# Performance work log

Measured on AMD Instinct MI355X. Metric: run time of the kernel, lower is better.

The kernel has to match this reference:

```python
import jax, jax.numpy as jnp
import numpy as np
from jax import lax

SHIFT = 32  # shift_range from init
EPS_NORM = 1e-12
EPS_MASK = 1e-6


def _l2_normalize_flat(x):
    # F.normalize(x.reshape(B,-1)): per-sample L2 normalize with eps 1e-12
    B = x.shape[0]
    flat = x.reshape(B, -1)
    n = jnp.linalg.norm(flat, axis=1, keepdims=True)
    return (flat / jnp.maximum(n, EPS_NORM)).reshape(x.shape)


def setup_inputs() -> dict:
    key = jax.random.key(0)
    k1, k2 = jax.random.split(key)
    grd_feature = jax.random.normal(k1, (8, 32, 32, 32), dtype=jnp.float32)
    sat_feature = jax.random.normal(k2, (8, 32, 128, 128), dtype=jnp.float32)
    return {"grd_feature": grd_feature, "sat_feature": sat_feature, "test_method": 1}


def reference(grd_feature, sat_feature, test_method):
    # test_method == 1 path (default); test_method in {0,1} only differ in divisor
    M, C, H_s, W_s = sat_feature.shape
    N, _, H, W = grd_feature.shape
    kH = min(H, H_s - 2 * SHIFT)
    kW = min(W, W_s - 2 * SHIFT)

    # center-crop ground template to (kH, kW) and L2-normalize per sample
    gh0, gw0 = H // 2 - kH // 2, W // 2 - kW // 2
    grd = grd_feature[:, :, gh0:gh0 + 2 * (kH // 2), gw0:gw0 + 2 * (kW // 2)]
    N_, _, H_k, W_k = grd.shape
    grd = _l2_normalize_flat(grd)

    # center-crop satellite to search region and L2-normalize per sample
    sh0 = H_s // 2 - SHIFT - kH // 2
    sw0 = W_s // 2 - SHIFT - kW // 2
    sat = sat_feature[:, :, sh0:sh0 + 2 * (SHIFT + kH // 2), sw0:sw0 + 2 * (SHIFT + kW // 2)]
    _, _, H_i, W_i = sat.shape
    sat = _l2_normalize_flat(sat)

    # all-pairs cross-correlation: corr[m, n, y, x] (torch grouped-conv on repeated sat
    # is equivalent to a plain VALID conv of sat with all N ground filters)
    corr = lax.conv_general_dilated(
        sat, grd, window_strides=(1, 1), padding='VALID',
        dimension_numbers=('NCHW', 'OIHW', 'NCHW'))  # [M, N, Ho, Wo]
    Ho, Wo = corr.shape[2], corr.shape[3]

    # sliding-window sum of |sat|^2 (avg_pool with divisor_override=1, summed over C)
    s2 = jnp.sum(sat * sat, axis=1)  # [M, H_i, W_i]
    partical = lax.reduce_window(s2, jnp.float32(0), lax.add,
                                 (1, H_k, W_k), (1, 1, 1), 'VALID')  # [M, Ho, Wo]
    if test_method == 0:
        denom = jnp.sqrt(partical)
    else:
        denom = partical
    corr = corr / jnp.maximum(denom[:, None], EPS_NORM)

    similarity_matrix = jnp.max(corr, axis=(2, 3))  # [M, N]

    # diagonal pairs (m == n): peak localization
    diag = jnp.diagonal(corr, axis1=0, axis2=1)        # [Ho, Wo, M]
    diag = jnp.transpose(diag, (2, 0, 1)).reshape(M, -1)
    max_index = jnp.argmax(diag, axis=-1)
    pos_h = max_index // Wo
    pos_w = max_index % Wo

    grd_mask = (jnp.abs(jnp.sum(grd, axis=1)) > EPS_MASK).astype(jnp.float32)  # [N, H_k, W_k]

    def place(ph, pw, gm):
        z = jnp.zeros((1, H_i, W_i), dtype=jnp.float32)
        return lax.dynamic_update_slice(z, gm[None], (0, ph, pw))

    mask = jax.vmap(place)(pos_h, pos_w, grd_mask)  # [M, 1, H_i, W_i]
    return similarity_matrix, mask
```

## Files before the change

### kernel.cpp

```cpp
#include <hip/hip_runtime.h>
#include <stdint.h>

typedef unsigned short u16;
typedef unsigned int u32;
typedef unsigned long long u64;
typedef __bf16 bf16x8 __attribute__((ext_vector_type(8)));
typedef float floatx4 __attribute__((ext_vector_type(4)));

#define DEVI static __device__ __forceinline__

DEVI u16 f2bf(float f) {
  uint32_t u = __builtin_bit_cast(uint32_t, f);
  u += 0x7FFFu + ((u >> 16) & 1u);
  return (u16)(u >> 16);
}
DEVI float bf2f(u16 b) { return __builtin_bit_cast(float, (uint32_t)b << 16); }

DEVI u32 encf(float f) {
  u32 u = __builtin_bit_cast(u32, f);
  return (u >> 31) ? ~u : (u | 0x80000000u);
}
DEVI float decf(u32 e) {
  u32 u = (e >> 31) ? (e & 0x7FFFFFFFu) : ~e;
  return __builtin_bit_cast(float, u);
}

DEVI float wred_sum(float v) {
  #pragma unroll
  for (int o = 32; o > 0; o >>= 1) v += __shfl_xor(v, o);
  return v;
}
DEVI float wred_max(float v) {
  #pragma unroll
  for (int o = 32; o > 0; o >>= 1) v = fmaxf(v, __shfl_xor(v, o));
  return v;
}

DEVI void cp16(const u16* g, u16* l) {
#if __has_builtin(__builtin_amdgcn_global_load_lds)
  __builtin_amdgcn_global_load_lds(
      (const __attribute__((address_space(1))) uint32_t*)g,
      (__attribute__((address_space(3))) uint32_t*)l, 16, 0, 0);
#else
  *(uint4*)l = *(const uint4*)g;
#endif
}

static constexpr size_t OFF_CORRP = 0;
static constexpr size_t OFF_SATT  = OFF_CORRP + (size_t)4*270400*4;
static constexpr size_t OFF_GRDP  = OFF_SATT + (size_t)8*4*96*96*8*2;
static constexpr size_t OFF_S2    = OFF_GRDP + (size_t)4*1024*16*8*2;
static constexpr size_t OFF_PART  = OFF_S2   + (size_t)73728*4;
static constexpr size_t OFF_NRMP  = OFF_PART + (size_t)33800*4;
static constexpr size_t OFF_GNRM  = OFF_NRMP + 768*4;
static constexpr size_t OFF_MASK  = OFF_GNRM + 32;
static constexpr size_t OFF_PMAX  = OFF_MASK + (size_t)8192*4;
static constexpr size_t OFF_CNT   = OFF_PMAX + 320*4;

__global__ __launch_bounds__(256) void k_prep(
    const float* __restrict__ grd, const float* __restrict__ sat,
    u16* __restrict__ sTh, u16* __restrict__ gP,
    float* __restrict__ s2, float* __restrict__ nrmp,
    float* __restrict__ gnrm, float* __restrict__ gmask,
    u32* __restrict__ cnts) {
  __shared__ float L[32*100];
  __shared__ float red[4];
  const int t = threadIdx.x;
  if (blockIdx.x < 768) {
    const int m = blockIdx.x / 96, y = blockIdx.x - (blockIdx.x / 96) * 96;
    #pragma unroll
    for (int k = 0; k < 3; ++k) {
      const int idx = k*256 + t;
      const int c = idx / 24, xq = idx - c*24;
      const float4 v = *(const float4*)(sat + (((size_t)m*32 + c)*128 + (16+y))*128 + 16 + xq*4);
      *(float4*)(&L[c*100 + xq*4]) = v;
    }
    __syncthreads();
    float ss = 0.f;
    if (t < 96) {
      #pragma unroll
      for (int c = 0; c < 32; ++c) { const float v = L[c*100 + t]; ss += v*v; }
      s2[(size_t)m*9216 + y*96 + t] = ss;
    }
    const float wsum = wred_sum(ss);
    if ((t & 63) == 0) red[t >> 6] = wsum;
    __syncthreads();
    if (t == 0) nrmp[m*96 + y] = red[0] + red[1] + red[2] + red[3];
    for (int idx = t; idx < 384; idx += 256) {
      const int cb = idx / 96, x = idx - cb*96;
      union { u16 us[8]; uint4 v4; } P;
      #pragma unroll
      for (int e = 0; e < 8; ++e) P.us[e] = f2bf(L[(cb*8+e)*100 + x]);
      *(uint4*)(&sTh[(((size_t)m*4+cb)*9216 + (size_t)y*96 + x)*8]) = P.v4;
    }
  } else if (blockIdx.x == 776) {
    if (t < 96) cnts[t] = (t == 72) ? 768u : 0u;
  } else {
    const int n = blockIdx.x - 768;
    float nn = 0.f, scs[4];
    #pragma unroll
    for (int it = 0; it < 4; ++it) {
      const int pidx = it*256 + t;
      float vals[32]; float sc = 0.f;
      #pragma unroll
      for (int c = 0; c < 32; ++c) {
        const float v = grd[((size_t)n*32 + c)*1024 + pidx];
        vals[c] = v; sc += v; nn += v*v;
      }
      scs[it] = sc;
      #pragma unroll
      for (int cb = 0; cb < 4; ++cb) {
        union { u16 us[8]; uint4 v4; } ph, pl;
        #pragma unroll
        for (int e = 0; e < 8; ++e) {
          const float v = vals[cb*8+e];
          const u16 h = f2bf(v); ph.us[e] = h; pl.us[e] = f2bf(v - bf2f(h));
        }
        const size_t o = ((size_t)cb*1024 + pidx)*128;
        *(uint4*)(&gP[o + (size_t)n*8])     = ph.v4;
        *(uint4*)(&gP[o + (size_t)(n+8)*8]) = pl.v4;
      }
    }
    const float tot = wred_sum(nn);
    if ((t & 63) == 0) red[t >> 6] = tot;
    __syncthreads();
    const float sum = red[0] + red[1] + red[2] + red[3];
    if (t == 0) gnrm[n] = sum;
    const float gn = fmaxf(sqrtf(sum), 1e-12f);
    const float thr = 1e-6f * gn;
    #pragma unroll
    for (int it = 0; it < 4; ++it)
      gmask[n*1024 + it*256 + t] = (fabsf(scs[it]) > thr) ? 1.f : 0.f;
  }
}

__global__ __launch_bounds__(256, 3) void k_conv(
    const u16* __restrict__ satT, const u16* __restrict__ gP,
    const float* __restrict__ s2, float* __restrict__ corr_p,
    float* __restrict__ part, u32* __restrict__ tick)
{
  __shared__ __align__(16) u16 patch[41*48*8];
  __shared__ u32 s_bi;

  const int tid = threadIdx.x;
  const int wave = tid >> 6, lane = tid & 63;
  const int pr = lane & 15, q = lane >> 4;

  u32 bi = blockIdx.x;
  for (;;) {
    if (bi < 72) {
      float* S  = (float*)patch;
      float* HS = S + 40*96;
      const int pm = (int)bi / 9, ysl = ((int)bi - pm*9)*8;
      const int nrows = (65 - ysl) < 8 ? (65 - ysl) : 8;
      const int scnt  = (96 - ysl) < 40 ? (96 - ysl) : 40;
      for (int idx = tid; idx < scnt*96; idx += 256)
        S[idx] = s2[(size_t)pm*9216 + (size_t)ysl*96 + idx];
      __syncthreads();
      const int hrows = nrows + 31;
      for (int idx = tid; idx < hrows*65; idx += 256) {
        const int r = idx / 65, xo = idx - r*65;
        const float* p = &S[r*96 + xo];
        float s = 0.f;
        #pragma unroll
        for (int j = 0; j < 32; ++j) s += p[j];
        HS[idx] = s;
      }
      __syncthreads();
      for (int idx = tid; idx < nrows*65; idx += 256) {
        const int r = idx / 65, xo = idx - r*65;
        float s = 0.f;
        #pragma unroll
        for (int i = 0; i < 32; ++i) s += HS[(r+i)*65 + xo];
        part[(size_t)pm*4225 + (size_t)(ysl+r)*65 + xo] = s;
      }
    } else if (bi >= 968) {
      const int e = (int)bi - 968;
      const int cb = e & 3;
      const int yt = (e >> 2) % 5;
      const int m  = e / 20;
      const int ybase = yt * 13;
      const size_t rowbase = ((size_t)(m*4 + cb) * 96 + ybase) * 96;
      for (int k = tid; k < 44*32; k += 256) {
        const int rho = k >> 5, px = k & 31;
        cp16(&satT[(rowbase + (size_t)rho*96 + 64 + px)*8], &patch[(size_t)k*8]);
      }
      asm volatile("s_waitcnt vmcnt(0)" ::: "memory");
      __syncthreads();
      const int prc = pr < 13 ? pr : 12;
      floatx4 acc = (floatx4){0.f, 0.f, 0.f, 0.f};
      #pragma unroll
      for (int jbi = 0; jbi < 2; ++jbi) {
        const int jb = wave*2 + jbi;
        const int px_e = jb*4 + q;
        const u16* bp = gP + ((size_t)cb*1024 + (size_t)(jb*4+q))*128 + (size_t)pr*8;
        uint4 Br[8];
        #pragma unroll
        for (int ii = 0; ii < 8; ++ii) Br[ii] = *(const uint4*)(bp + (size_t)ii*4096);
        uint4 Ah[8];
        #pragma unroll
        for (int s = 0; s < 6; ++s)
          Ah[s] = *(const uint4*)(&patch[((size_t)(prc + s)*32 + px_e)*8]);
        #pragma unroll
        for (int i = 0; i < 32; ++i) {
          if (i < 26)
            Ah[(i+6)&7] = *(const uint4*)(&patch[((size_t)(prc + i + 6)*32 + px_e)*8]);
          const bf16x8 bf = __builtin_bit_cast(bf16x8, Br[i&7]);
          if (i < 24)
            Br[(i+8)&7] = *(const uint4*)(bp + (size_t)(i+8)*4096);
          acc = __builtin_amdgcn_mfma_f32_16x16x32_bf16(
              __builtin_bit_cast(bf16x8, Ah[i&7]), bf, acc, 0, 0, 0);
        }
      }
      float v4[4];
      #pragma unroll
      for (int k = 0; k < 4; ++k) v4[k] = acc[k] + __shfl_xor(acc[k], 8);
      __syncthreads();
      float* red = (float*)patch;
      #pragma unroll
      for (int k = 0; k < 4; ++k) red[((size_t)wave*64 + lane)*5 + k] = v4[k];
      __syncthreads();
      if (wave == 0 && pr < 8) {
        #pragma unroll
        for (int k = 0; k < 4; ++k) {
          const int yoff = q*4 + k;
          if (yoff < 13) {
            float s = 0.f;
            #pragma unroll
            for (int w = 0; w < 4; ++w) s += red[((size_t)w*64 + lane)*5 + k];
            corr_p[(size_t)cb*270400 + ((size_t)(m*8+pr)*65 + (ybase+yoff))*65 + 64] = s;
          }
        }
      }
    } else {
      int bb = (int)bi - 72;
      const int cb = bb & 3; bb >>= 2;
      const int xt = bb & 3; bb >>= 2;
      const int yt = bb % 7;
      const int m  = bb / 7;
      const int x0 = xt*16;

      if (yt < 6) {
        const int y0 = yt*10;
        const size_t rowbase = ((size_t)(m*4 + cb) * 96 + y0) * 96;
        for (int k = tid; k < 41*48; k += 256) {
          const int rho = k / 48, px = k - (k/48)*48;
          cp16(&satT[(rowbase + (size_t)rho*96 + x0 + px)*8], &patch[(size_t)k*8]);
        }
        asm volatile("s_waitcnt vmcnt(0)" ::: "memory");
        __syncthreads();

        floatx4 acc[10];
        #pragma unroll
        for (int r = 0; r < 10; ++r) acc[r] = (floatx4){0.f, 0.f, 0.f, 0.f};

        #pragma unroll
        for (int jbi = 0; jbi < 2; ++jbi) {
          const int jb = wave*2 + jbi;
          const int apx = pr + jb*4 + q;
          const u16* bp = gP + ((size_t)cb*1024 + (size_t)(jb*4+q))*128 + (size_t)pr*8;

          uint4 Br[8];
          #pragma unroll
          for (int ii = 0; ii < 8; ++ii) Br[ii] = *(const uint4*)(bp + (size_t)ii*4096);
          uint4 Ah[12];
          #pragma unroll
          for (int s = 0; s < 12; ++s) Ah[s] = *(const uint4*)(&patch[((size_t)s*48 + apx)*8]);

          #pragma unroll
          for (int i = 0; i < 32; ++i) {
            const bf16x8 bf = __builtin_bit_cast(bf16x8, Br[i&7]);
            if (i < 24)
              Br[(i+8)&7] = *(const uint4*)(bp + (size_t)(i+8)*4096);
            __builtin_amdgcn_s_setprio(1);
            #pragma unroll
            for (int r = 0; r < 10; ++r)
              acc[r] = __builtin_amdgcn_mfma_f32_16x16x32_bf16(
                  __builtin_bit_cast(bf16x8, Ah[(i+r)%12]), bf, acc[r], 0, 0, 0);
            __builtin_amdgcn_s_setprio(0);
            if (i < 29)
              Ah[(i+12)%12] = *(const uint4*)(&patch[((size_t)(i+12)*48 + apx)*8]);
          }
        }

        float* red = (float*)patch;
        #pragma unroll
        for (int half = 0; half < 2; ++half) {
          __syncthreads();
          #pragma unroll
          for (int u = 0; u < 20; ++u)
            red[((size_t)wave*64 + lane)*21 + u] = acc[half*5 + (u>>2)][u&3];
          __syncthreads();
          if (pr < 8) {
            const int fw = wave;
            #pragma unroll
            for (int r = 0; r < 5; ++r) {
              float s = 0.f;
              #pragma unroll
              for (int w = 0; w < 4; ++w)
                s += red[((size_t)w*64 + lane)*21 + r*4 + fw]
                   + red[((size_t)w*64 + (lane^8))*21 + r*4 + fw];
              const int x = x0 + q*4 + fw;
              corr_p[(size_t)cb*270400 + ((size_t)(m*8+pr)*65 + (y0 + half*5 + r))*65 + x] = s;
            }
          }
        }
      } else {
        const int y0 = 60;
        const size_t rowbase = ((size_t)(m*4 + cb) * 96 + y0) * 96;
        for (int k = tid; k < 36*48; k += 256) {
          const int rho = k / 48, px = k - (k/48)*48;
          cp16(&satT[(rowbase + (size_t)rho*96 + x0 + px)*8], &patch[(size_t)k*8]);
        }
        asm volatile("s_waitcnt vmcnt(0)" ::: "memory");
        __syncthreads();

        floatx4 acc[5];
        #pragma unroll
        for (int r = 0; r < 5; ++r) acc[r] = (floatx4){0.f, 0.f, 0.f, 0.f};

        #pragma unroll
        for (int jbi = 0; jbi < 2; ++jbi) {
          const int jb = wave*2 + jbi;
          const int apx = pr + jb*4 + q;
          const u16* bp = gP + ((size_t)cb*1024 + (size_t)(jb*4+q))*128 + (size_t)pr*8;

          uint4 Br[8];
          #pragma unroll
          for (int ii = 0; ii < 8; ++ii) Br[ii] = *(const uint4*)(bp + (size_t)ii*4096);
          uint4 Ah[8];
          #pragma unroll
          for (int s = 0; s < 6; ++s) Ah[s] = *(const uint4*)(&patch[((size_t)s*48 + apx)*8]);

          #pragma unroll
          for (int i = 0; i < 32; ++i) {
            if (i < 30)
              Ah[(i+6)&7] = *(const uint4*)(&patch[((size_t)(i+6)*48 + apx)*8]);
            const bf16x8 bf = __builtin_bit_cast(bf16x8, Br[i&7]);
            if (i < 24)
              Br[(i+8)&7] = *(const uint4*)(bp + (size_t)(i+8)*4096);
            __builtin_amdgcn_s_setprio(1);
            #pragma unroll
            for (int r = 0; r < 5; ++r)
              acc[r] = __builtin_amdgcn_mfma_f32_16x16x32_bf16(
                  __builtin_bit_cast(bf16x8, Ah[(i+r)&7]), bf, acc[r], 0, 0, 0);
            __builtin_amdgcn_s_setprio(0);
          }
        }

        __syncthreads();
        float* red = (float*)patch;
        #pragma unroll
        for (int u = 0; u < 20; ++u)
          red[((size_t)wave*64 + lane)*21 + u] = acc[u>>2][u&3];
        __syncthreads();
        if (pr < 8) {
          const int fw = wave;
          #pragma unroll
          for (int r = 0; r < 5; ++r) {
            float s = 0.f;
            #pragma unroll
            for (int w = 0; w < 4; ++w)
              s += red[((size_t)w*64 + lane)*21 + r*4 + fw]
                 + red[((size_t)w*64 + (lane^8))*21 + r*4 + fw];
            const int x = x0 + q*4 + fw;
            corr_p[(size_t)cb*270400 + ((size_t)(m*8+pr)*65 + (y0+r))*65 + x] = s;
          }
        }
      }
    }

    __syncthreads();
    if (tid == 0) s_bi = atomicAdd(tick, 1u);
    __syncthreads();
    bi = s_bi;
    if (bi >= 1128) return;
  }
}

__global__ __launch_bounds__(256) void k_post(
    const float* __restrict__ corr_p, const float* __restrict__ part,
    const float* __restrict__ nrmp, const float* __restrict__ gnrm,
    const int* __restrict__ tm, const float* __restrict__ grd,
    const float* __restrict__ sat, const float* __restrict__ gmask,
    u32* __restrict__ pmaxE, u32* __restrict__ grpcnt,
    u64* __restrict__ bestu, float* __restrict__ out)
{
  __shared__ float red[8];
  __shared__ int s_last;
  __shared__ int fidx[128];
  __shared__ u32 fcnt;
  __shared__ u64 s_bk;

  const int bi = blockIdx.x;
  const int m = bi / 40, n = (bi / 5) & 7, yc = bi % 5, g = m*8 + n;
  const int t = threadIdx.x;
  const int wv = t >> 6, ln = t & 63;
  const bool diag = (m == n);

  float v0 = (t < 96) ? nrmp[m*96 + t] : 0.f;
  v0 = wred_sum(v0);
  if (ln == 0) red[wv] = v0;
  __syncthreads();
  const float snrm2 = red[0] + red[1] + red[2] + red[3];
  const float srn = 1.f / fmaxf(sqrtf(snrm2), 1e-12f);
  const float grn = 1.f / fmaxf(sqrtf(gnrm[n]), 1e-12f);
  const float cscale = grn * srn, pscale = srn * srn;
  const int method = tm[0];

  const float* cp = corr_p + (size_t)g*4225;
  const float* pp = part + (size_t)m*4225;
  const int i0 = yc*845, i1 = i0 + 845;
  float vv[4];
  float bestv = -3.4e38f;
  #pragma unroll
  for (int k = 0; k < 4; ++k) {
    const int idx = i0 + k*256 + t;
    float v = -3.4e38f;
    if (idx < i1) {
      const float c = cp[idx] + cp[idx+270400] + cp[idx+540800] + cp[idx+811200];
      const float pt = pp[idx] * pscale;
      float denom = (method == 0) ? sqrtf(pt) : pt;
      denom = fmaxf(denom, 1e-12f);
      v = c * cscale / denom;
    }
    vv[k] = v;
    bestv = fmaxf(bestv, v);
  }
  __syncthreads();
  const float bw = wred_max(bestv);
  if (ln == 0) red[wv] = bw;
  __syncthreads();
  const float bmax = fmaxf(fmaxf(red[0], red[1]), fmaxf(red[2], red[3]));
  if (t == 0) atomicExch(&pmaxE[bi], encf(bmax));

  if (diag) {
    if (t == 0) fcnt = 0u;
    __syncthreads();
    const float lthr = bmax - 3e-3f;
    #pragma unroll
    for (int k = 0; k < 4; ++k) {
      const int idx = i0 + k*256 + t;
      if (idx < i1 && vv[k] >= lthr) {
        const u32 s = atomicAdd(&fcnt, 1u);
        if (s < 128) fidx[s] = idx;
      }
    }
    __syncthreads();
    const int nf = (int)(fcnt < 128u ? fcnt : 128u);
    u64 bestKey = 0ULL;
    const int c = t >> 3, s8 = t & 7;
    for (int ci = 0; ci < nf; ++ci) {
      const int idx = fidx[ci];
      const int y = idx / 65, x = idx - y*65;
      float a = 0.f;
      #pragma unroll
      for (int ii = 0; ii < 4; ++ii) {
        const int i = s8 + ii*8;
        const float* gr = grd + ((size_t)n*32 + c)*1024 + i*32;
        const float* sr = sat + (((size_t)n*32 + c)*128 + (16 + y + i))*128 + (16 + x);
        #pragma unroll
        for (int j = 0; j < 32; ++j) a += gr[j] * sr[j];
      }
      a = wred_sum(a);
      if (ln == 0) red[wv] = a;
      __syncthreads();
      if (t == 0) {
        const float tot = red[0] + red[1] + red[2] + red[3];
        const float pt = part[(size_t)n*4225 + idx] * pscale;
        float denom = (method == 0) ? sqrtf(pt) : pt;
        denom = fmaxf(denom, 1e-12f);
        const float v = tot * cscale / denom;
        const u64 key = ((u64)encf(v) << 32) | (u64)(0xFFFFFFFFu - (u32)idx);
        if (key > bestKey) bestKey = key;
      }
      __syncthreads();
    }
    if (t == 0 && nf > 0) atomicMax(&bestu[n], bestKey);
    __threadfence();
  }

  __syncthreads();
  if (t == 0) s_last = (atomicAdd(&grpcnt[g], 1u) == 4u) ? 1 : 0;
  __syncthreads();
  if (!s_last) return;

  if (t < 5) red[t] = decf(atomicOr(&pmaxE[g*5 + t], 0u));
  __syncthreads();
  const float gmax = fmaxf(fmaxf(fmaxf(red[0], red[1]), fmaxf(red[2], red[3])), red[4]);
  if (t == 0) out[g] = gmax;
  if (!diag) return;

  if (t == 0) s_bk = atomicAdd(&bestu[n], 0ULL);
  __syncthreads();
  const int bix = (int)(0xFFFFFFFFu - (u32)s_bk);
  const int ph = bix / 65, pw = bix - (bix/65)*65;
  for (int p = t; p < 9216; p += 256) {
    const int yy = p / 96, xx = p - yy*96;
    float val = 0.f;
    if (yy >= ph && yy < ph+32 && xx >= pw && xx < pw+32)
      val = gmask[n*1024 + (yy-ph)*32 + (xx-pw)];
    out[64 + (size_t)n*9216 + p] = val;
  }
}

extern "C" void kernel_launch(void* const* d_in, const int* in_sizes, int n_in,
                              void* d_out, int out_size, void* d_ws, size_t ws_size,
                              hipStream_t stream) {
  const float* grd = (const float*)d_in[0];
  const float* sat = (const float*)d_in[1];
  const int*   tm  = (const int*)d_in[2];
  float* out = (float*)d_out;
  char* ws = (char*)d_ws;

  float* corrp = (float*)(ws + OFF_CORRP);
  u16*   sTh   = (u16*)(ws + OFF_SATT);
  u16*   gP    = (u16*)(ws + OFF_GRDP);
  float* s2    = (float*)(ws + OFF_S2);
  float* part  = (float*)(ws + OFF_PART);
  float* nrmp  = (float*)(ws + OFF_NRMP);
  float* gnrm  = (float*)(ws + OFF_GNRM);
  float* gmask = (float*)(ws + OFF_MASK);
  u32*   pmaxE = (u32*)(ws + OFF_PMAX);
  u32*   cnts  = (u32*)(ws + OFF_CNT);
  u32*   tick  = cnts + 72;
  u64*   bestu = (u64*)(ws + OFF_CNT + 320);

  k_prep<<<777, 256, 0, stream>>>(grd, sat, sTh, gP, s2, nrmp, gnrm, gmask, cnts);
  k_conv<<<768, 256, 0, stream>>>(sTh, gP, s2, corrp, part, tick);
  k_post<<<320, 256, 0, stream>>>(corrp, part, nrmp, gnrm, tm, grd, sat, gmask,
                                  pmaxE, cnts, bestu, out);
}
```

Baseline: 154.1 us.

## Move diagonal peak refinement into separate kernel using global-threshold candidate filtering

Diagonal blocks in k_post no longer recompute exact fp32 correlations for every near-max candidate of their own row chunk. Instead they push packed (value, index) candidates to a global per-sample list. A new k_refine kernel then filters those candidates against the whole-map maximum and recomputes only the survivors, one candidate per wavefront with vectorized ground loads. This removes the serialized per-candidate block-wide reductions on the critical tail of k_post and cuts redundant refinements, at the cost of an extra kernel launch and a global candidate buffer capped at 128 entries per sample.

```diff
diff --git a/kernel.cpp b/kernel.cpp
--- a/kernel.cpp
+++ b/kernel.cpp
@@ -19,10 +19,6 @@
 DEVI u32 encf(float f) {
   u32 u = __builtin_bit_cast(u32, f);
   return (u >> 31) ? ~u : (u | 0x80000000u);
-}
-DEVI float decf(u32 e) {
-  u32 u = (e >> 31) ? (e & 0x7FFFFFFFu) : ~e;
-  return __builtin_bit_cast(float, u);
 }
 
 DEVI float wred_sum(float v) {
@@ -56,6 +52,7 @@
 static constexpr size_t OFF_MASK  = OFF_GNRM + 32;
 static constexpr size_t OFF_PMAX  = OFF_MASK + (size_t)8192*4;
 static constexpr size_t OFF_CNT   = OFF_PMAX + 320*4;
+static constexpr size_t OFF_CAND  = OFF_CNT  + 512;
 
 __global__ __launch_bounds__(256) void k_prep(
     const float* __restrict__ grd, const float* __restrict__ sat,
@@ -381,16 +378,13 @@
 __global__ __launch_bounds__(256) void k_post(
     const float* __restrict__ corr_p, const float* __restrict__ part,
     const float* __restrict__ nrmp, const float* __restrict__ gnrm,
-    const int* __restrict__ tm, const float* __restrict__ grd,
-    const float* __restrict__ sat, const float* __restrict__ gmask,
+    const int* __restrict__ tm,
     u32* __restrict__ pmaxE, u32* __restrict__ grpcnt,
-    u64* __restrict__ bestu, float* __restrict__ out)
+    u32* __restrict__ candcnt, u64* __restrict__ cand,
+    float* __restrict__ out)
 {
   __shared__ float red[8];
   __shared__ int s_last;
-  __shared__ int fidx[128];
-  __shared__ u32 fcnt;
-  __shared__ u64 s_bk;
 
   const int bi = blockIdx.x;
   const int m = bi / 40, n = (bi / 5) & 7, yc = bi % 5, g = m*8 + n;
@@ -435,65 +429,114 @@
   if (t == 0) atomicExch(&pmaxE[bi], encf(bmax));
 
   if (diag) {
-    if (t == 0) fcnt = 0u;
-    __syncthreads();
     const float lthr = bmax - 3e-3f;
     #pragma unroll
     for (int k = 0; k < 4; ++k) {
       const int idx = i0 + k*256 + t;
       if (idx < i1 && vv[k] >= lthr) {
-        const u32 s = atomicAdd(&fcnt, 1u);
-        if (s < 128) fidx[s] = idx;
-      }
-    }
-    __syncthreads();
-    const int nf = (int)(fcnt < 128u ? fcnt : 128u);
-    u64 bestKey = 0ULL;
-    const int c = t >> 3, s8 = t & 7;
-    for (int ci = 0; ci < nf; ++ci) {
-      const int idx = fidx[ci];
-      const int y = idx / 65, x = idx - y*65;
-      float a = 0.f;
-      #pragma unroll
-      for (int ii = 0; ii < 4; ++ii) {
-        const int i = s8 + ii*8;
-        const float* gr = grd + ((size_t)n*32 + c)*1024 + i*32;
-        const float* sr = sat + (((size_t)n*32 + c)*128 + (16 + y + i))*128 + (16 + x);
-        #pragma unroll
-        for (int j = 0; j < 32; ++j) a += gr[j] * sr[j];
-      }
-      a = wred_sum(a);
-      if (ln == 0) red[wv] = a;
-      __syncthreads();
-      if (t == 0) {
-        const float tot = red[0] + red[1] + red[2] + red[3];
-        const float pt = part[(size_t)n*4225 + idx] * pscale;
-        float denom = (method == 0) ? sqrtf(pt) : pt;
-        denom = fmaxf(denom, 1e-12f);
-        const float v = tot * cscale / denom;
-        const u64 key = ((u64)encf(v) << 32) | (u64)(0xFFFFFFFFu - (u32)idx);
-        if (key > bestKey) bestKey = key;
-      }
-      __syncthreads();
-    }
-    if (t == 0 && nf > 0) atomicMax(&bestu[n], bestKey);
-    __threadfence();
-  }
-
+        const u32 s = atomicAdd(&candcnt[n], 1u);
+        if (s < 128)
+          atomicExch(&cand[n*128 + s],
+                     ((u64)__builtin_bit_cast(u32, vv[k]) << 32) | (u32)idx);
+      }
+    }
+  }
   __syncthreads();
   if (t == 0) s_last = (atomicAdd(&grpcnt[g], 1u) == 4u) ? 1 : 0;
   __syncthreads();
   if (!s_last) return;
 
-  if (t < 5) red[t] = decf(atomicOr(&pmaxE[g*5 + t], 0u));
+  if (t < 5) red[t] = __builtin_bit_cast(float, 0u);
+  if (t < 5) {
+    const u32 e = atomicOr(&pmaxE[g*5 + t], 0u);
+    const u32 u = (e >> 31) ? (e & 0x7FFFFFFFu) : ~e;
+    red[t] = __builtin_bit_cast(float, u);
+  }
   __syncthreads();
   const float gmax = fmaxf(fmaxf(fmaxf(red[0], red[1]), fmaxf(red[2], red[3])), red[4]);
   if (t == 0) out[g] = gmax;
-  if (!diag) return;
-
-  if (t == 0) s_bk = atomicAdd(&bestu[n], 0ULL);
-  __syncthreads();
-  const int bix = (int)(0xFFFFFFFFu - (u32)s_bk);
+}
+
+__global__ __launch_bounds__(256) void k_refine(
+    const float* __restrict__ part, const float* __restrict__ nrmp,
+    const float* __restrict__ gnrm, const int* __restrict__ tm,
+    const float* __restrict__ grd, const float* __restrict__ sat,
+    const float* __restrict__ gmask,
+    const u32* __restrict__ candcnt, const u64* __restrict__ cand,
+    float* __restrict__ out)
+{
+  __shared__ float red[4];
+  __shared__ int fidx[128];
+  __shared__ u32 fcnt;
+  __shared__ u64 wkey[4];
+
+  const int n = blockIdx.x;
+  const int t = threadIdx.x;
+  const int wv = t >> 6, ln = t & 63;
+
+  float v0 = (t < 96) ? nrmp[n*96 + t] : 0.f;
+  v0 = wred_sum(v0);
+  if (ln == 0) red[wv] = v0;
+  if (t == 0) fcnt = 0u;
+  __syncthreads();
+  const float snrm2 = red[0] + red[1] + red[2] + red[3];
+  const float srn = 1.f / fmaxf(sqrtf(snrm2), 1e-12f);
+  const float grn = 1.f / fmaxf(sqrtf(gnrm[n]), 1e-12f);
+  const float cscale = grn * srn, pscale = srn * srn;
+  const int method = tm[0];
+
+  const float gmax = out[9*n];
+  const float thr = gmax - 3e-3f;
+
+  u32 nc = candcnt[n]; if (nc > 128u) nc = 128u;
+  if (t < (int)nc) {
+    const u64 pk = cand[n*128 + t];
+    const float vf = __builtin_bit_cast(float, (u32)(pk >> 32));
+    const int idx = (int)(u32)pk;
+    if (vf >= thr) {
+      const u32 s = atomicAdd(&fcnt, 1u);
+      if (s < 128u) fidx[s] = idx;
+    }
+  }
+  __syncthreads();
+  if (t == 0 && fcnt == 0u) { fidx[0] = 0; fcnt = 1u; }
+  __syncthreads();
+  const int nf = (int)(fcnt < 128u ? fcnt : 128u);
+
+  u64 bestKey = 0ULL;
+  for (int ci = wv; ci < nf; ci += 4) {
+    const int idx = fidx[ci];
+    const int y = idx / 65, x = idx - y*65;
+    float a = 0.f;
+    #pragma unroll
+    for (int k = 0; k < 16; ++k) {
+      const int p = ln + 64*k;
+      const int c = p >> 5, i = p & 31;
+      const float4* gr4 = (const float4*)(grd + ((size_t)n*32 + c)*1024 + i*32);
+      const float* sr = sat + (((size_t)n*32 + c)*128 + (16 + y + i))*128 + (16 + x);
+      #pragma unroll
+      for (int j4 = 0; j4 < 8; ++j4) {
+        const float4 g4 = gr4[j4];
+        a += g4.x*sr[j4*4] + g4.y*sr[j4*4+1] + g4.z*sr[j4*4+2] + g4.w*sr[j4*4+3];
+      }
+    }
+    a = wred_sum(a);
+    if (ln == 0) {
+      const float pt = part[(size_t)n*4225 + idx] * pscale;
+      float denom = (method == 0) ? sqrtf(pt) : pt;
+      denom = fmaxf(denom, 1e-12f);
+      const float v = a * cscale / denom;
+      const u64 key = ((u64)encf(v) << 32) | (u64)(0xFFFFFFFFu - (u32)idx);
+      if (key > bestKey) bestKey = key;
+    }
+  }
+  if (ln == 0) wkey[wv] = bestKey;
+  __syncthreads();
+  u64 bk = wkey[0];
+  if (wkey[1] > bk) bk = wkey[1];
+  if (wkey[2] > bk) bk = wkey[2];
+  if (wkey[3] > bk) bk = wkey[3];
+  const int bix = (int)(0xFFFFFFFFu - (u32)bk);
   const int ph = bix / 65, pw = bix - (bix/65)*65;
   for (int p = t; p < 9216; p += 256) {
     const int yy = p / 96, xx = p - yy*96;
@@ -523,11 +566,14 @@
   float* gmask = (float*)(ws + OFF_MASK);
   u32*   pmaxE = (u32*)(ws + OFF_PMAX);
   u32*   cnts  = (u32*)(ws + OFF_CNT);
+  u32*   candcnt = cnts + 64;
   u32*   tick  = cnts + 72;
-  u64*   bestu = (u64*)(ws + OFF_CNT + 320);
+  u64*   cand  = (u64*)(ws + OFF_CAND);
 
   k_prep<<<777, 256, 0, stream>>>(grd, sat, sTh, gP, s2, nrmp, gnrm, gmask, cnts);
   k_conv<<<768, 256, 0, stream>>>(sTh, gP, s2, corrp, part, tick);
-  k_post<<<320, 256, 0, stream>>>(corrp, part, nrmp, gnrm, tm, grd, sat, gmask,
-                                  pmaxE, cnts, bestu, out);
-}
+  k_post<<<320, 256, 0, stream>>>(corrp, part, nrmp, gnrm, tm,
+                                  pmaxE, cnts, candcnt, cand, out);
+  k_refine<<<8, 256, 0, stream>>>(part, nrmp, gnrm, tm, grd, sat, gmask,
+                                  candcnt, cand, out);
+}
```

Result: slower. 158.7 us (+3.0%).
